# Kernel optimization log

Hardware: AMD Instinct MI355X
Metric: run time of the kernel (lower is better)

Reference implementation:

```python
import jax, jax.numpy as jnp
import numpy as np

B, N, K = 4096, 87, 87


def setup_inputs() -> dict:
    key = jax.random.key(0)
    ks = jax.random.split(key, 6)
    x = jax.random.normal(ks[0], (B, N, N), dtype=jnp.float32)
    evals = jax.random.uniform(ks[1], (B, K), dtype=jnp.float32)
    evecs = jax.random.normal(ks[2], (B, N, K), dtype=jnp.float32)
    # learned per-node diffusion times (torch inits to 0, clamped to 1e-8;
    # use small positive values to exercise the exp decay)
    diffusion_time = jax.random.uniform(ks[3], (N,), dtype=jnp.float32) * 0.1
    # MiniMLP: single Linear(2*N -> N)
    lim = 1.0 / np.sqrt(2 * N)
    W = jax.random.uniform(ks[4], (N, 2 * N), minval=-lim, maxval=lim, dtype=jnp.float32)
    b = jax.random.uniform(ks[5], (N,), minval=-lim, maxval=lim, dtype=jnp.float32)
    return {"x": x, "evals": evals, "evecs": evecs,
            "diffusion_time": diffusion_time, "W": W, "b": b}


def reference(x, evals, evecs, diffusion_time, W, b):
    # clamp diffusion times (torch does this in-place on .data)
    t = jnp.maximum(diffusion_time, 1e-8)                     # (N,)
    # expa[b,i,m] = exp(-t_i * eval[b,m])
    expa = jnp.exp(-t[None, :, None] * evals[:, None, :])     # (B,N,K)
    # kernel[b,i,j] = sum_m evec[b,i,m] * expa[b,i,m] * evec[b,j,m]
    # (equivalent to the diag_embed + triple matmul + diagonal in the torch code)
    kernel = jnp.einsum('bim,bjm->bij', evecs * expa, evecs)  # (B,N,N)
    x_diffuse = jnp.concatenate([x, kernel], axis=2)          # (B,N,2N)
    return x_diffuse @ W.T + b                                # (B,N,N)
```

## Files before the change

### kernel.cpp

```cpp
#include <hip/hip_runtime.h>
#include <hip/hip_bf16.h>
#include <math.h>

#define NN    87
#define NN2   (NN * NN)
#define EPW   92
#define EF1   (NN * EPW + 8)
#define SDN   (NN * EPW + 4)
#define WPH   104
#define WPANEL (96 * WPH)
#define NT    256
#define GRIDB 512

#define PAD_N    8360
#define WS_W     0
#define WS_EPAD  (2 * WPANEL * 2)
#define WS_XPAD  (WS_EPAD + PAD_N * 4)
#define WS_NEED  (WS_XPAD + PAD_N * 4)

typedef __attribute__((ext_vector_type(8))) short bf16x8;
typedef __attribute__((ext_vector_type(4))) short bf16x4;
typedef __attribute__((ext_vector_type(4))) float f32x4;
typedef float f32x4u __attribute__((ext_vector_type(4), aligned(4)));

__device__ __forceinline__ short f2bf(float f) {
    __hip_bfloat16 h = __float2bfloat16(f);
    return *(short*)&h;
}

__device__ __forceinline__ void gl16(const float* g, float* l) {
    __builtin_amdgcn_global_load_lds(
        (const __attribute__((address_space(1))) void*)g,
        (__attribute__((address_space(3))) void*)l, 16, 0, 0);
}

__global__ void prep(const float* __restrict__ W, const float* __restrict__ evecs,
                     const float* __restrict__ x, int B, char* __restrict__ ws)
{
    int idx = (int)blockIdx.x * NT + (int)threadIdx.x;
    short* wpp = (short*)(ws + WS_W);
    float* ep  = (float*)(ws + WS_EPAD);
    float* xp  = (float*)(ws + WS_XPAD);
    if (idx < 2 * WPANEL) {
        int p = idx / WPANEL, rem = idx - p * WPANEL;
        int r = rem / WPH, c = rem - r * WPH;
        short v = 0;
        if (r < NN && c < NN) v = f2bf(W[r * (2 * NN) + p * NN + c]);
        wpp[idx] = v;
    }
    int i2 = idx - 2 * WPANEL;
    if (i2 >= 0 && i2 < PAD_N) ep[i2] = (i2 < NN2) ? evecs[(size_t)(B - 1) * NN2 + i2] : 0.f;
    int i3 = i2 - PAD_N;
    if (i3 >= 0 && i3 < PAD_N) xp[i3] = (i3 < NN2) ? x[(size_t)(B - 1) * NN2 + i3] : 0.f;
}

template <bool WS>
__device__ __forceinline__ bf16x8 wload(const short* __restrict__ wp,
                                        const float* __restrict__ gW,
                                        int panel, int jrow, int jcl, int k0, bool tailKs)
{
    if constexpr (WS) {
        return *(const bf16x8*)&wp[panel * WPANEL + jrow * WPH + k0];
    } else {
        float v[8];
        if (!tailKs) {
            f32x4u a  = *(const f32x4u*)(gW + jcl * (2 * NN) + panel * NN + k0);
            f32x4u b4 = *(const f32x4u*)(gW + jcl * (2 * NN) + panel * NN + k0 + 4);
            v[0] = a.x; v[1] = a.y; v[2] = a.z; v[3] = a.w;
            v[4] = b4.x; v[5] = b4.y; v[6] = b4.z; v[7] = b4.w;
        } else {
            #pragma unroll
            for (int q = 0; q < 8; ++q) {
                int k = k0 + q;
                v[q] = (k < NN) ? gW[jcl * (2 * NN) + panel * NN + k] : 0.f;
            }
        }
        bf16x8 o;
        #pragma unroll
        for (int q = 0; q < 8; ++q) o[q] = f2bf(v[q]);
        return o;
    }
}

template <bool WS>
__device__ __forceinline__ void stageE(const float* __restrict__ Eb, float* __restrict__ sEb,
                                       int tid, int wave, int lane)
{
    if constexpr (WS) {
        for (int vc = wave; vc < 32; vc += 4) {
            int p   = vc * 256 + lane * 4;
            int row = p / EPW;
            int col = p - row * EPW;
            const float* g = Eb + row * NN + col;
            if (vc < 31) gl16(g, &sEb[vc * 256]);
            else if (lane < 17) gl16(g, &sEb[vc * 256]);
        }
    } else {
        for (int u = tid; u < NN * 22; u += NT) {
            int r = u / 22, sg = u - r * 22, c = sg * 4;
            const float* pE = Eb + r * NN + c;
            if (sg < 21) *(f32x4*)&sEb[r * EPW + c] = *(const f32x4u*)pE;
            else { f32x4 t; t.x = pE[0]; t.y = pE[1]; t.z = pE[2]; t.w = 0.f;
                   *(f32x4*)&sEb[r * EPW + c] = t; }
        }
        for (int u = tid; u < NN * 4; u += NT) {
            int r = u >> 2, c = 88 + (u & 3);
            sEb[r * EPW + c] = 0.f;
        }
    }
}

template <bool WS>
__global__ __launch_bounds__(NT, 2)
void fused(const float* __restrict__ gx, const float* __restrict__ gevals,
           const float* __restrict__ gevecs, const float* __restrict__ dtime,
           const float* __restrict__ gW, const float* __restrict__ bias,
           const char* __restrict__ ws, int B, int gridB, float* __restrict__ out)
{
    __shared__ __align__(16) float sE[2][EF1];
    __shared__ __align__(16) short sD[SDN];
    __shared__ float sLam[2][96];

    const int tid  = (int)threadIdx.x;
    const int lane = tid & 63;
    const int wave = tid >> 6;
    const int l15  = lane & 15;
    const int lk   = lane >> 4;
    const int i0   = (wave >> 1) * 48;
    const int j0   = (wave & 1) * 48;

    const short* wp   = nullptr;
    const float* epad = nullptr;
    const float* xpad = nullptr;
    if constexpr (WS) {
        wp   = (const short*)(ws + WS_W);
        epad = (const float*)(ws + WS_EPAD);
        xpad = (const float*)(ws + WS_XPAD);
    }

    int iw[3], jw[3], iru[3], jru[3];
    float tr_[3];
    #pragma unroll
    for (int r = 0; r < 3; ++r) {
        iw[r]  = i0 + 16 * r + l15;
        jw[r]  = j0 + 16 * r + l15;
        iru[r] = (iw[r] < NN) ? iw[r] : NN - 1;
        jru[r] = (jw[r] < NN) ? jw[r] : NN - 1;
        tr_[r] = fmaxf(dtime[iru[r]], 1e-8f);
    }

    bf16x8 wfx[3][3], wfd[3][3];
    #pragma unroll
    for (int ks = 0; ks < 3; ++ks)
        #pragma unroll
        for (int wr = 0; wr < 3; ++wr) {
            wfx[ks][wr] = wload<WS>(wp, gW, 0, jw[wr], jru[wr], ks * 32 + lk * 8, ks == 2);
            wfd[ks][wr] = wload<WS>(wp, gW, 1, jw[wr], jru[wr], ks * 32 + lk * 8, ks == 2);
        }
    float bjv[3][4];
    #pragma unroll
    for (int wr = 0; wr < 3; ++wr) {
        const int jb = j0 + 16 * wr + lk * 4;
        if (jb + 3 < NN) {
            f32x4u t = *(const f32x4u*)(bias + jb);
            bjv[wr][0] = t.x; bjv[wr][1] = t.y; bjv[wr][2] = t.z; bjv[wr][3] = t.w;
        } else {
            #pragma unroll
            for (int q = 0; q < 4; ++q) bjv[wr][q] = (jb + q < NN) ? bias[jb + q] : 0.f;
        }
    }

    if (tid < 8) { sE[0][NN * EPW + tid] = 0.f; sE[1][NN * EPW + tid] = 0.f; }
    if (tid < 4) sD[NN * EPW + tid] = 0;

    const int b0 = (int)blockIdx.x;
    {
        const float* Eb = gevecs + (size_t)b0 * NN2;
        if (WS && b0 == B - 1) Eb = epad;
        stageE<WS>(Eb, sE[0], tid, wave, lane);
        if (tid < 96) sLam[0][tid] = (tid < NN) ? gevals[(size_t)b0 * NN + tid] : 3e38f;
    }
    __syncthreads();

    for (int it = 0, b = b0; b < B; ++it, b += gridB) {
        const int  p  = it & 1;
        const int  bn = b + gridB;
        const bool hn = bn < B;

        if (hn) {
            const float* Ebn = gevecs + (size_t)bn * NN2;
            if (WS && bn == B - 1) Ebn = epad;
            stageE<WS>(Ebn, sE[1 - p], tid, wave, lane);
        }
        float lamn = 3e38f;
        if (hn && tid < NN) lamn = gevals[(size_t)bn * NN + tid];

        f32x4 acc1[3][3];
        #pragma unroll
        for (int c = 0; c < 3; ++c)
            #pragma unroll
            for (int r = 0; r < 3; ++r) acc1[c][r] = (f32x4){0.f, 0.f, 0.f, 0.f};

        const float* sEp = sE[p];
        #pragma unroll
        for (int ks = 0; ks < 3; ++ks) {
            const int k0 = ks * 32 + lk * 8;
            f32x4 la  = *(const f32x4*)&sLam[p][k0];
            f32x4 lb4 = *(const f32x4*)&sLam[p][k0 + 4];
            float l8_[8] = {la.x, la.y, la.z, la.w, lb4.x, lb4.y, lb4.z, lb4.w};

            bf16x8 ef[3], af[3];
            #pragma unroll
            for (int c = 0; c < 3; ++c) {
                f32x4 lo = *(const f32x4*)&sEp[jru[c] * EPW + k0];
                f32x4 hi = *(const f32x4*)&sEp[jru[c] * EPW + k0 + 4];
                #pragma unroll
                for (int q = 0; q < 4; ++q) { ef[c][q] = f2bf(lo[q]); ef[c][q + 4] = f2bf(hi[q]); }
            }
            #pragma unroll
            for (int r = 0; r < 3; ++r) {
                f32x4 lo = *(const f32x4*)&sEp[iru[r] * EPW + k0];
                f32x4 hi = *(const f32x4*)&sEp[iru[r] * EPW + k0 + 4];
                #pragma unroll
                for (int q = 0; q < 4; ++q) {
                    af[r][q]     = f2bf(lo[q] * __expf(-tr_[r] * l8_[q]));
                    af[r][q + 4] = f2bf(hi[q] * __expf(-tr_[r] * l8_[q + 4]));
                }
            }
            #pragma unroll
            for (int c = 0; c < 3; ++c)
                #pragma unroll
                for (int r = 0; r < 3; ++r)
                    acc1[c][r] = __builtin_amdgcn_mfma_f32_16x16x32_bf16(ef[c], af[r], acc1[c][r], 0, 0, 0);
        }

        const float* xbb = gx + (size_t)b * NN2;
        bool xvec = true;
        if (b == B - 1) { if (WS) xbb = xpad; else xvec = false; }
        float xr[3][3][8];
        #pragma unroll
        for (int xc = 0; xc < 3; ++xc)
            #pragma unroll
            for (int ks = 0; ks < 3; ++ks) {
                const int off = iru[xc] * NN + ks * 32 + lk * 8;
                if (xvec) {
                    f32x4u a  = *(const f32x4u*)(xbb + off);
                    f32x4u b4 = *(const f32x4u*)(xbb + off + 4);
                    xr[xc][ks][0] = a.x;  xr[xc][ks][1] = a.y;
                    xr[xc][ks][2] = a.z;  xr[xc][ks][3] = a.w;
                    xr[xc][ks][4] = b4.x; xr[xc][ks][5] = b4.y;
                    xr[xc][ks][6] = b4.z; xr[xc][ks][7] = b4.w;
                } else {
                    #pragma unroll
                    for (int q = 0; q < 8; ++q) {
                        int o = off + q;
                        xr[xc][ks][q] = xbb[(o < NN2) ? o : (NN2 - 1)];
                    }
                }
            }

        #pragma unroll
        for (int c = 0; c < 3; ++c) {
            const int jb = j0 + 16 * c + lk * 4;
            if (jb < EPW) {
                #pragma unroll
                for (int r = 0; r < 3; ++r) {
                    if (iw[r] < NN) {
                        bf16x4 v = {f2bf(acc1[c][r][0]), f2bf(acc1[c][r][1]),
                                    f2bf(acc1[c][r][2]), f2bf(acc1[c][r][3])};
                        *(bf16x4*)&sD[iw[r] * EPW + jb] = v;
                    }
                }
            }
        }
        if (hn && tid < 96) sLam[1 - p][tid] = (tid < NN) ? lamn : 3e38f;

        asm volatile("s_waitcnt lgkmcnt(0)" ::: "memory");
        __builtin_amdgcn_s_barrier();
        __builtin_amdgcn_sched_barrier(0);

        f32x4 acc2[3][3];
        #pragma unroll
        for (int wr = 0; wr < 3; ++wr)
            #pragma unroll
            for (int xc = 0; xc < 3; ++xc) {
                acc2[wr][xc][0] = bjv[wr][0]; acc2[wr][xc][1] = bjv[wr][1];
                acc2[wr][xc][2] = bjv[wr][2]; acc2[wr][xc][3] = bjv[wr][3];
            }

        #pragma unroll
        for (int ks = 0; ks < 3; ++ks) {
            bf16x8 xf[3];
            #pragma unroll
            for (int xc = 0; xc < 3; ++xc)
                #pragma unroll
                for (int q = 0; q < 8; ++q) xf[xc][q] = f2bf(xr[xc][ks][q]);
            #pragma unroll
            for (int wr = 0; wr < 3; ++wr)
                #pragma unroll
                for (int xc = 0; xc < 3; ++xc)
                    acc2[wr][xc] = __builtin_amdgcn_mfma_f32_16x16x32_bf16(
                        wfx[ks][wr], xf[xc], acc2[wr][xc], 0, 0, 0);
        }
        #pragma unroll
        for (int ks = 0; ks < 3; ++ks) {
            const int k0 = ks * 32 + lk * 8;
            bf16x8 df[3];
            #pragma unroll
            for (int xc = 0; xc < 3; ++xc) {
                bf16x4 lo = *(const bf16x4*)&sD[iru[xc] * EPW + k0];
                bf16x4 hi = *(const bf16x4*)&sD[iru[xc] * EPW + k0 + 4];
                #pragma unroll
                for (int q = 0; q < 4; ++q) { df[xc][q] = lo[q]; df[xc][q + 4] = hi[q]; }
            }
            #pragma unroll
            for (int wr = 0; wr < 3; ++wr)
                #pragma unroll
                for (int xc = 0; xc < 3; ++xc)
                    acc2[wr][xc] = __builtin_amdgcn_mfma_f32_16x16x32_bf16(
                        wfd[ks][wr], df[xc], acc2[wr][xc], 0, 0, 0);
        }

        {
            float* __restrict__ gb = out + (size_t)b * NN2;
            #pragma unroll
            for (int wr = 0; wr < 3; ++wr) {
                const int jb = j0 + 16 * wr + lk * 4;
                #pragma unroll
                for (int xc = 0; xc < 3; ++xc) {
                    const int i = iw[xc];
                    if (i < NN) {
                        if (jb + 3 < NN) {
                            f32x4u v;
                            v.x = acc2[wr][xc][0]; v.y = acc2[wr][xc][1];
                            v.z = acc2[wr][xc][2]; v.w = acc2[wr][xc][3];
                            *(f32x4u*)&gb[i * NN + jb] = v;
                        } else {
                            #pragma unroll
                            for (int q = 0; q < 4; ++q)
                                if (jb + q < NN) gb[i * NN + jb + q] = acc2[wr][xc][q];
                        }
                    }
                }
            }
        }

        if (hn) __syncthreads();
    }
}

extern "C" void kernel_launch(void* const* d_in, const int* in_sizes, int n_in,
                              void* d_out, int out_size, void* d_ws, size_t ws_size,
                              hipStream_t stream)
{
    const float* x     = (const float*)d_in[0];
    const float* evals = (const float*)d_in[1];
    const float* evecs = (const float*)d_in[2];
    const float* dtime = (const float*)d_in[3];
    const float* W     = (const float*)d_in[4];
    const float* bias  = (const float*)d_in[5];
    float* out = (float*)d_out;

    const int B = in_sizes[1] / NN;
    const int gridB = (B < GRIDB) ? B : GRIDB;

    if (ws_size >= (size_t)WS_NEED) {
        const int prep_elems = 2 * WPANEL + 2 * PAD_N;
        prep<<<(prep_elems + NT - 1) / NT, NT, 0, stream>>>(W, evecs, x, B, (char*)d_ws);
        fused<true><<<dim3(gridB), dim3(NT), 0, stream>>>(x, evals, evecs, dtime, W, bias,
                                                          (const char*)d_ws, B, gridB, out);
    } else {
        fused<false><<<dim3(gridB), dim3(NT), 0, stream>>>(x, evals, evecs, dtime, W, bias,
                                                           nullptr, B, gridB, out);
    }
}
```

Measured before the change: 88.54 us.

## Split fused kernel work across twelve waves with one i-tile per wave

Blocks grow from 4 to 12 waves (768 threads), and the grid shrinks from 512 to 256 blocks. Each wave now owns a single 16-row i-tile instead of three, which cuts per-thread accumulators, the x loads and the MFMA count per wave. The intent is lower register pressure and more waves in flight to hide latency. The trade-off is one block per CU, more barrier participants, and each wave still redundantly converting the shared ef/W fragments.

```diff
diff --git a/kernel.cpp b/kernel.cpp
--- a/kernel.cpp
+++ b/kernel.cpp
@@ -10,7 +10,8 @@
 #define WPH   104
 #define WPANEL (96 * WPH)
 #define NT    256
-#define GRIDB 512
+#define FT    768
+#define GRIDB 256
 
 #define PAD_N    8360
 #define WS_W     0
@@ -87,7 +88,7 @@
                                        int tid, int wave, int lane)
 {
     if constexpr (WS) {
-        for (int vc = wave; vc < 32; vc += 4) {
+        for (int vc = wave; vc < 32; vc += 12) {
             int p   = vc * 256 + lane * 4;
             int row = p / EPW;
             int col = p - row * EPW;
@@ -96,14 +97,14 @@
             else if (lane < 17) gl16(g, &sEb[vc * 256]);
         }
     } else {
-        for (int u = tid; u < NN * 22; u += NT) {
+        for (int u = tid; u < NN * 22; u += FT) {
             int r = u / 22, sg = u - r * 22, c = sg * 4;
             const float* pE = Eb + r * NN + c;
             if (sg < 21) *(f32x4*)&sEb[r * EPW + c] = *(const f32x4u*)pE;
             else { f32x4 t; t.x = pE[0]; t.y = pE[1]; t.z = pE[2]; t.w = 0.f;
                    *(f32x4*)&sEb[r * EPW + c] = t; }
         }
-        for (int u = tid; u < NN * 4; u += NT) {
+        for (int u = tid; u < NN * 4; u += FT) {
             int r = u >> 2, c = 88 + (u & 3);
             sEb[r * EPW + c] = 0.f;
         }
@@ -111,7 +112,7 @@
 }
 
 template <bool WS>
-__global__ __launch_bounds__(NT, 2)
+__global__ __launch_bounds__(FT, 1)
 void fused(const float* __restrict__ gx, const float* __restrict__ gevals,
            const float* __restrict__ gevecs, const float* __restrict__ dtime,
            const float* __restrict__ gW, const float* __restrict__ bias,
@@ -126,7 +127,7 @@
     const int wave = tid >> 6;
     const int l15  = lane & 15;
     const int lk   = lane >> 4;
-    const int i0   = (wave >> 1) * 48;
+    const int i0   = (wave >> 1) * 16;
     const int j0   = (wave & 1) * 48;
 
     const short* wp   = nullptr;
@@ -138,15 +139,14 @@
         xpad = (const float*)(ws + WS_XPAD);
     }
 
-    int iw[3], jw[3], iru[3], jru[3];
-    float tr_[3];
+    const int iw  = i0 + l15;
+    const int iru = (iw < NN) ? iw : NN - 1;
+    const float tr_ = fmaxf(dtime[iru], 1e-8f);
+    int jw[3], jru[3];
     #pragma unroll
-    for (int r = 0; r < 3; ++r) {
-        iw[r]  = i0 + 16 * r + l15;
-        jw[r]  = j0 + 16 * r + l15;
-        iru[r] = (iw[r] < NN) ? iw[r] : NN - 1;
-        jru[r] = (jw[r] < NN) ? jw[r] : NN - 1;
-        tr_[r] = fmaxf(dtime[iru[r]], 1e-8f);
+    for (int c = 0; c < 3; ++c) {
+        jw[c]  = j0 + 16 * c + l15;
+        jru[c] = (jw[c] < NN) ? jw[c] : NN - 1;
     }
 
     bf16x8 wfx[3][3], wfd[3][3];
@@ -195,11 +195,9 @@
         float lamn = 3e38f;
         if (hn && tid < NN) lamn = gevals[(size_t)bn * NN + tid];
 
-        f32x4 acc1[3][3];
-        #pragma unroll
-        for (int c = 0; c < 3; ++c)
-            #pragma unroll
-            for (int r = 0; r < 3; ++r) acc1[c][r] = (f32x4){0.f, 0.f, 0.f, 0.f};
+        f32x4 acc1[3];
+        #pragma unroll
+        for (int c = 0; c < 3; ++c) acc1[c] = (f32x4){0.f, 0.f, 0.f, 0.f};
 
         const float* sEp = sE[p];
         #pragma unroll
@@ -209,7 +207,7 @@
             f32x4 lb4 = *(const f32x4*)&sLam[p][k0 + 4];
             float l8_[8] = {la.x, la.y, la.z, la.w, lb4.x, lb4.y, lb4.z, lb4.w};
 
-            bf16x8 ef[3], af[3];
+            bf16x8 ef[3], af;
             #pragma unroll
             for (int c = 0; c < 3; ++c) {
                 f32x4 lo = *(const f32x4*)&sEp[jru[c] * EPW + k0];
@@ -217,60 +215,48 @@
                 #pragma unroll
                 for (int q = 0; q < 4; ++q) { ef[c][q] = f2bf(lo[q]); ef[c][q + 4] = f2bf(hi[q]); }
             }
-            #pragma unroll
-            for (int r = 0; r < 3; ++r) {
-                f32x4 lo = *(const f32x4*)&sEp[iru[r] * EPW + k0];
-                f32x4 hi = *(const f32x4*)&sEp[iru[r] * EPW + k0 + 4];
+            {
+                f32x4 lo = *(const f32x4*)&sEp[iru * EPW + k0];
+                f32x4 hi = *(const f32x4*)&sEp[iru * EPW + k0 + 4];
                 #pragma unroll
                 for (int q = 0; q < 4; ++q) {
-                    af[r][q]     = f2bf(lo[q] * __expf(-tr_[r] * l8_[q]));
-                    af[r][q + 4] = f2bf(hi[q] * __expf(-tr_[r] * l8_[q + 4]));
+                    af[q]     = f2bf(lo[q] * __expf(-tr_ * l8_[q]));
+                    af[q + 4] = f2bf(hi[q] * __expf(-tr_ * l8_[q + 4]));
                 }
             }
             #pragma unroll
             for (int c = 0; c < 3; ++c)
-                #pragma unroll
-                for (int r = 0; r < 3; ++r)
-                    acc1[c][r] = __builtin_amdgcn_mfma_f32_16x16x32_bf16(ef[c], af[r], acc1[c][r], 0, 0, 0);
+                acc1[c] = __builtin_amdgcn_mfma_f32_16x16x32_bf16(ef[c], af, acc1[c], 0, 0, 0);
         }
 
         const float* xbb = gx + (size_t)b * NN2;
         bool xvec = true;
         if (b == B - 1) { if (WS) xbb = xpad; else xvec = false; }
-        float xr[3][3][8];
-        #pragma unroll
-        for (int xc = 0; xc < 3; ++xc)
-            #pragma unroll
-            for (int ks = 0; ks < 3; ++ks) {
-                const int off = iru[xc] * NN + ks * 32 + lk * 8;
-                if (xvec) {
-                    f32x4u a  = *(const f32x4u*)(xbb + off);
-                    f32x4u b4 = *(const f32x4u*)(xbb + off + 4);
-                    xr[xc][ks][0] = a.x;  xr[xc][ks][1] = a.y;
-                    xr[xc][ks][2] = a.z;  xr[xc][ks][3] = a.w;
-                    xr[xc][ks][4] = b4.x; xr[xc][ks][5] = b4.y;
-                    xr[xc][ks][6] = b4.z; xr[xc][ks][7] = b4.w;
-                } else {
-                    #pragma unroll
-                    for (int q = 0; q < 8; ++q) {
-                        int o = off + q;
-                        xr[xc][ks][q] = xbb[(o < NN2) ? o : (NN2 - 1)];
-                    }
+        float xr[3][8];
+        #pragma unroll
+        for (int ks = 0; ks < 3; ++ks) {
+            const int off = iru * NN + ks * 32 + lk * 8;
+            if (xvec) {
+                f32x4u a  = *(const f32x4u*)(xbb + off);
+                f32x4u b4 = *(const f32x4u*)(xbb + off + 4);
+                xr[ks][0] = a.x;  xr[ks][1] = a.y;  xr[ks][2] = a.z;  xr[ks][3] = a.w;
+                xr[ks][4] = b4.x; xr[ks][5] = b4.y; xr[ks][6] = b4.z; xr[ks][7] = b4.w;
+            } else {
+                #pragma unroll
+                for (int q = 0; q < 8; ++q) {
+                    int o = off + q;
+                    xr[ks][q] = xbb[(o < NN2) ? o : (NN2 - 1)];
                 }
             }
+        }
 
         #pragma unroll
         for (int c = 0; c < 3; ++c) {
             const int jb = j0 + 16 * c + lk * 4;
-            if (jb < EPW) {
-                #pragma unroll
-                for (int r = 0; r < 3; ++r) {
-                    if (iw[r] < NN) {
-                        bf16x4 v = {f2bf(acc1[c][r][0]), f2bf(acc1[c][r][1]),
-                                    f2bf(acc1[c][r][2]), f2bf(acc1[c][r][3])};
-                        *(bf16x4*)&sD[iw[r] * EPW + jb] = v;
-                    }
-                }
+            if (jb < EPW && iw < NN) {
+                bf16x4 v = {f2bf(acc1[c][0]), f2bf(acc1[c][1]),
+                            f2bf(acc1[c][2]), f2bf(acc1[c][3])};
+                *(bf16x4*)&sD[iw * EPW + jb] = v;
             }
         }
         if (hn && tid < 96) sLam[1 - p][tid] = (tid < NN) ? lamn : 3e38f;
@@ -279,68 +265,53 @@
         __builtin_amdgcn_s_barrier();
         __builtin_amdgcn_sched_barrier(0);
 
-        f32x4 acc2[3][3];
-        #pragma unroll
-        for (int wr = 0; wr < 3; ++wr)
-            #pragma unroll
-            for (int xc = 0; xc < 3; ++xc) {
-                acc2[wr][xc][0] = bjv[wr][0]; acc2[wr][xc][1] = bjv[wr][1];
-                acc2[wr][xc][2] = bjv[wr][2]; acc2[wr][xc][3] = bjv[wr][3];
-            }
+        f32x4 acc2[3];
+        #pragma unroll
+        for (int wr = 0; wr < 3; ++wr) {
+            acc2[wr][0] = bjv[wr][0]; acc2[wr][1] = bjv[wr][1];
+            acc2[wr][2] = bjv[wr][2]; acc2[wr][3] = bjv[wr][3];
+        }
 
         #pragma unroll
         for (int ks = 0; ks < 3; ++ks) {
-            bf16x8 xf[3];
-            #pragma unroll
-            for (int xc = 0; xc < 3; ++xc)
-                #pragma unroll
-                for (int q = 0; q < 8; ++q) xf[xc][q] = f2bf(xr[xc][ks][q]);
+            bf16x8 xf;
+            #pragma unroll
+            for (int q = 0; q < 8; ++q) xf[q] = f2bf(xr[ks][q]);
             #pragma unroll
             for (int wr = 0; wr < 3; ++wr)
-                #pragma unroll
-                for (int xc = 0; xc < 3; ++xc)
-                    acc2[wr][xc] = __builtin_amdgcn_mfma_f32_16x16x32_bf16(
-                        wfx[ks][wr], xf[xc], acc2[wr][xc], 0, 0, 0);
+                acc2[wr] = __builtin_amdgcn_mfma_f32_16x16x32_bf16(
+                    wfx[ks][wr], xf, acc2[wr], 0, 0, 0);
         }
         #pragma unroll
         for (int ks = 0; ks < 3; ++ks) {
             const int k0 = ks * 32 + lk * 8;
-            bf16x8 df[3];
-            #pragma unroll
-            for (int xc = 0; xc < 3; ++xc) {
-                bf16x4 lo = *(const bf16x4*)&sD[iru[xc] * EPW + k0];
-                bf16x4 hi = *(const bf16x4*)&sD[iru[xc] * EPW + k0 + 4];
+            bf16x8 df;
+            {
+                bf16x4 lo = *(const bf16x4*)&sD[iru * EPW + k0];
+                bf16x4 hi = *(const bf16x4*)&sD[iru * EPW + k0 + 4];
                 #pragma unroll
-                for (int q = 0; q < 4; ++q) { df[xc][q] = lo[q]; df[xc][q + 4] = hi[q]; }
+                for (int q = 0; q < 4; ++q) { df[q] = lo[q]; df[q + 4] = hi[q]; }
             }
             #pragma unroll
             for (int wr = 0; wr < 3; ++wr)
-                #pragma unroll
-                for (int xc = 0; xc < 3; ++xc)
-                    acc2[wr][xc] = __builtin_amdgcn_mfma_f32_16x16x32_bf16(
-                        wfd[ks][wr], df[xc], acc2[wr][xc], 0, 0, 0);
-        }
-
-        {
+                acc2[wr] = __builtin_amdgcn_mfma_f32_16x16x32_bf16(
+                    wfd[ks][wr], df, acc2[wr], 0, 0, 0);
+        }
+
+        if (iw < NN) {
             float* __restrict__ gb = out + (size_t)b * NN2;
             #pragma unroll
             for (int wr = 0; wr < 3; ++wr) {
                 const int jb = j0 + 16 * wr + lk * 4;
-                #pragma unroll
-                for (int xc = 0; xc < 3; ++xc) {
-                    const int i = iw[xc];
-                    if (i < NN) {
-                        if (jb + 3 < NN) {
-                            f32x4u v;
-                            v.x = acc2[wr][xc][0]; v.y = acc2[wr][xc][1];
-                            v.z = acc2[wr][xc][2]; v.w = acc2[wr][xc][3];
-                            *(f32x4u*)&gb[i * NN + jb] = v;
-                        } else {
-                            #pragma unroll
-                            for (int q = 0; q < 4; ++q)
-                                if (jb + q < NN) gb[i * NN + jb + q] = acc2[wr][xc][q];
-                        }
-                    }
+                if (jb + 3 < NN) {
+                    f32x4u v;
+                    v.x = acc2[wr][0]; v.y = acc2[wr][1];
+                    v.z = acc2[wr][2]; v.w = acc2[wr][3];
+                    *(f32x4u*)&gb[iw * NN + jb] = v;
+                } else {
+                    #pragma unroll
+                    for (int q = 0; q < 4; ++q)
+                        if (jb + q < NN) gb[iw * NN + jb + q] = acc2[wr][q];
                 }
             }
         }
@@ -367,10 +338,10 @@
     if (ws_size >= (size_t)WS_NEED) {
         const int prep_elems = 2 * WPANEL + 2 * PAD_N;
         prep<<<(prep_elems + NT - 1) / NT, NT, 0, stream>>>(W, evecs, x, B, (char*)d_ws);
-        fused<true><<<dim3(gridB), dim3(NT), 0, stream>>>(x, evals, evecs, dtime, W, bias,
+        fused<true><<<dim3(gridB), dim3(FT), 0, stream>>>(x, evals, evecs, dtime, W, bias,
                                                           (const char*)d_ws, B, gridB, out);
     } else {
-        fused<false><<<dim3(gridB), dim3(NT), 0, stream>>>(x, evals, evecs, dtime, W, bias,
+        fused<false><<<dim3(gridB), dim3(FT), 0, stream>>>(x, evals, evecs, dtime, W, bias,
                                                            nullptr, B, gridB, out);
     }
 }
```

Result: no change. 86.89 us (-1.9%).
